# Kernel optimization log

Measured on AMD Instinct MI355X. Metric: run time of the kernel, lower is better.

Reference implementation:

```python
import jax, jax.numpy as jnp
import numpy as np

N_NODES = 100000
N_EDGES = 1600000
F_IN = 128
F_OUT = 64


def setup_inputs() -> dict:
    key = jax.random.key(0)
    k0, k1, k2, k3, k4, k5 = jax.random.split(key, 6)
    stdv = 1.0 / np.sqrt(F_OUT)
    x = jax.random.normal(k0, (N_NODES, F_IN), dtype=jnp.float32)
    edge_src = jax.random.randint(k1, (N_EDGES,), 0, N_NODES, dtype=jnp.int32)
    edge_dst = jax.random.randint(k2, (N_EDGES,), 0, N_NODES, dtype=jnp.int32)
    # normalized adjacency values (all positive, like D^-1/2 A D^-1/2 entries)
    edge_weight = jax.random.uniform(k3, (N_EDGES,), dtype=jnp.float32)
    weight = jax.random.uniform(k4, (F_IN, F_OUT), dtype=jnp.float32, minval=-stdv, maxval=stdv)
    bias = jax.random.uniform(k5, (F_OUT,), dtype=jnp.float32, minval=-stdv, maxval=stdv)
    return {"x": x, "edge_weight": edge_weight, "weight": weight, "bias": bias,
            "edge_src": edge_src, "edge_dst": edge_dst}


def reference(x, edge_weight, weight, bias, edge_src, edge_dst):
    # support = X @ W  -- dense GEMM [N, F_in] x [F_in, F_out]
    support = x @ weight
    # spmm(adj, support): adj in COO form; gather source rows, scale by edge value,
    # scatter-add into destination rows.
    msgs = support[edge_src] * edge_weight[:, None]          # [E, F_out]
    out = jax.ops.segment_sum(msgs, edge_dst, num_segments=x.shape[0])
    return out + bias
```

## Files before the change

kernel.cpp:

```cpp
#include <hip/hip_runtime.h>
#include <hip/hip_bf16.h>

#define F_IN 128
#define F_OUT 64
#define BUCKET_SHIFT 7
#define BUCKET_NODES 128
#define BUCKET_CAP 2880
#define CNT_STRIDE 16
#define NB_MAX 800
#define SCAT_CHUNK 8192
#define P1_GEMM_ROWS 64
#define LDK 136

typedef __attribute__((ext_vector_type(8))) short bf16x8;
typedef __attribute__((ext_vector_type(4))) float f32x4;

__device__ inline short bf16_bits(float f) {
  __hip_bfloat16 h = __float2bfloat16(f);
  return *reinterpret_cast<short*>(&h);
}

union Phase1Smem {
  struct { short Bs[F_OUT][LDK]; } g;
  struct { int lhist[NB_MAX]; int lcur[NB_MAX]; int ldst[SCAT_CHUNK]; } s;
};

__global__ __launch_bounds__(512, 6) void gcn_phase1_kernel(
    const float* __restrict__ x, const float* __restrict__ w,
    __hip_bfloat16* __restrict__ support,
    const int* __restrict__ esrc, const int* __restrict__ edst,
    const float* __restrict__ ew, int* __restrict__ bcount,
    int2* __restrict__ region, int n_nodes, int n_edges, int nb,
    int n_scat_blocks) {
  __shared__ Phase1Smem sm;
  const int tid = threadIdx.x;

  if ((int)blockIdx.x < n_scat_blocks) {
    const int e0 = blockIdx.x * SCAT_CHUNK;
    const int e1 = min(e0 + SCAT_CHUNK, n_edges);
    const int n_local = e1 - e0;

    for (int i = tid; i < nb; i += 512) sm.s.lhist[i] = 0;
    __syncthreads();
    for (int i = tid; i < n_local; i += 512) {
      const int d = edst[e0 + i];
      sm.s.ldst[i] = d;
      atomicAdd(&sm.s.lhist[d >> BUCKET_SHIFT], 1);
    }
    __syncthreads();
    for (int b = tid; b < nb; b += 512) {
      const int c = sm.s.lhist[b];
      sm.s.lcur[b] = c ? atomicAdd(&bcount[b * CNT_STRIDE], c) : 0;
    }
    __syncthreads();
    for (int i = tid; i < n_local; i += 512) {
      const int d = sm.s.ldst[i];
      const int b = d >> BUCKET_SHIFT;
      const int pos = atomicAdd(&sm.s.lcur[b], 1);
      if (pos < BUCKET_CAP) {
        region[(size_t)b * BUCKET_CAP + pos] =
            make_int2((esrc[e0 + i] << BUCKET_SHIFT) | (d & (BUCKET_NODES - 1)),
                      __float_as_int(ew[e0 + i]));
      }
    }
  } else {
    const int gbid = (int)blockIdx.x - n_scat_blocks;
    const int block_row = gbid * P1_GEMM_ROWS;

#pragma unroll
    for (int i = 0; i < F_IN * F_OUT / 512; ++i) {
      const int idx = tid + i * 512;
      sm.g.Bs[idx & 63][idx >> 6] = bf16_bits(w[idx]);
    }

    const int lane = tid & 63;
    const int wid = tid >> 6;
    const int wr0 = (wid >> 1) * 16;
    const int wc0 = (wid & 1) * 32;
    const int m = lane & 15;
    const int quad = lane >> 4;
    const int row = block_row + wr0 + m;

    bf16x8 afrag[4];
    if (row < n_nodes) {
      const float4* xr = (const float4*)(x + (size_t)row * F_IN);
#pragma unroll
      for (int ks = 0; ks < 4; ++ks) {
        const float4 v0 = xr[ks * 8 + quad * 2];
        const float4 v1 = xr[ks * 8 + quad * 2 + 1];
        bf16x8 a;
        a[0] = bf16_bits(v0.x); a[1] = bf16_bits(v0.y);
        a[2] = bf16_bits(v0.z); a[3] = bf16_bits(v0.w);
        a[4] = bf16_bits(v1.x); a[5] = bf16_bits(v1.y);
        a[6] = bf16_bits(v1.z); a[7] = bf16_bits(v1.w);
        afrag[ks] = a;
      }
    } else {
#pragma unroll
      for (int ks = 0; ks < 4; ++ks) afrag[ks] = (bf16x8)0;
    }
    __syncthreads();

    f32x4 acc0 = {0.f, 0.f, 0.f, 0.f};
    f32x4 acc1 = {0.f, 0.f, 0.f, 0.f};
#pragma unroll
    for (int ks = 0; ks < 4; ++ks) {
      const int ko = ks * 32 + quad * 8;
      const bf16x8 b0 = *(const bf16x8*)&sm.g.Bs[wc0 + m][ko];
      const bf16x8 b1 = *(const bf16x8*)&sm.g.Bs[wc0 + 16 + m][ko];
      acc0 = __builtin_amdgcn_mfma_f32_16x16x32_bf16(afrag[ks], b0, acc0, 0, 0, 0);
      acc1 = __builtin_amdgcn_mfma_f32_16x16x32_bf16(afrag[ks], b1, acc1, 0, 0, 0);
    }
#pragma unroll
    for (int r = 0; r < 4; ++r) {
      const int orow = block_row + wr0 + quad * 4 + r;
      if (orow < n_nodes) {
        __hip_bfloat16* op = support + (size_t)orow * F_OUT;
        op[wc0 + m]      = __float2bfloat16(acc0[r]);
        op[wc0 + 16 + m] = __float2bfloat16(acc1[r]);
      }
    }
  }
}

__global__ __launch_bounds__(512, 6) void gcn_sort_agg_kernel(
    const __hip_bfloat16* __restrict__ support,
    const int2* __restrict__ region, const int* __restrict__ bcount,
    const float* __restrict__ bias, float* __restrict__ out, int n_nodes) {
  __shared__ int2 outb[BUCKET_CAP];
  __shared__ int hist[BUCKET_NODES];
  __shared__ int nbeg[BUCKET_NODES];
  __shared__ int lcur[BUCKET_NODES];
  const int b = blockIdx.x;
  const int tid = threadIdx.x;
  const int lane = tid & 63;

  int cnt = bcount[b * CNT_STRIDE];
  cnt = (cnt < BUCKET_CAP ? cnt : BUCKET_CAP);
  const int2* reg = region + (size_t)b * BUCKET_CAP;

  for (int i = tid; i < BUCKET_NODES; i += 512) hist[i] = 0;
  __syncthreads();
  for (int i = tid; i < cnt; i += 512) {
    atomicAdd(&hist[reg[i].x & (BUCKET_NODES - 1)], 1);
  }
  __syncthreads();
  if (tid < 64) {
    const int v0 = hist[lane];
    const int v1 = hist[64 + lane];
    int s0 = v0;
#pragma unroll
    for (int off = 1; off < 64; off <<= 1) {
      const int t = __shfl_up(s0, off, 64);
      if (lane >= off) s0 += t;
    }
    const int tot0 = __shfl(s0, 63, 64);
    int s1 = v1;
#pragma unroll
    for (int off = 1; off < 64; off <<= 1) {
      const int t = __shfl_up(s1, off, 64);
      if (lane >= off) s1 += t;
    }
    s1 += tot0;
    nbeg[lane] = s0 - v0;
    nbeg[64 + lane] = s1 - v1;
    lcur[lane] = s0 - v0;
    lcur[64 + lane] = s1 - v1;
  }
  __syncthreads();
  for (int i = tid; i < cnt; i += 512) {
    const int2 p = reg[i];
    const int pos = atomicAdd(&lcur[p.x & (BUCKET_NODES - 1)], 1);
    outb[pos] = make_int2(p.x >> BUCKET_SHIFT, p.y);
  }
  __syncthreads();

  const int wid = tid >> 6;
  const int r = lane >> 4;
  const int c4 = (lane & 15) * 4;
  const ushort* sup = (const ushort*)support;
  const float4 b4 = *(const float4*)(bias + c4);
  for (int nl = wid * 16; nl < wid * 16 + 16; ++nl) {
    const int g = (b << BUCKET_SHIFT) + nl;
    if (g >= n_nodes) break;
    const int s = nbeg[nl];
    const int e = lcur[nl];
    f32x4 acc0 = {0.f, 0.f, 0.f, 0.f};
    f32x4 acc1 = {0.f, 0.f, 0.f, 0.f};
    for (int j = s; j < e; j += 8) {
      const int jr0 = j + r;
      const int jr1 = j + 4 + r;
      const bool va = jr0 < e;
      const bool vb = jr1 < e;
      const int2 m0 = outb[va ? jr0 : e - 1];
      const int2 m1 = outb[vb ? jr1 : e - 1];
      const float w0 = va ? __int_as_float(m0.y) : 0.f;
      const float w1 = vb ? __int_as_float(m1.y) : 0.f;
      const uint2 d0 = *(const uint2*)(sup + (size_t)m0.x * F_OUT + c4);
      const uint2 d1 = *(const uint2*)(sup + (size_t)m1.x * F_OUT + c4);
      acc0[0] = fmaf(__uint_as_float(d0.x << 16), w0, acc0[0]);
      acc0[1] = fmaf(__uint_as_float(d0.x & 0xffff0000u), w0, acc0[1]);
      acc0[2] = fmaf(__uint_as_float(d0.y << 16), w0, acc0[2]);
      acc0[3] = fmaf(__uint_as_float(d0.y & 0xffff0000u), w0, acc0[3]);
      acc1[0] = fmaf(__uint_as_float(d1.x << 16), w1, acc1[0]);
      acc1[1] = fmaf(__uint_as_float(d1.x & 0xffff0000u), w1, acc1[1]);
      acc1[2] = fmaf(__uint_as_float(d1.y << 16), w1, acc1[2]);
      acc1[3] = fmaf(__uint_as_float(d1.y & 0xffff0000u), w1, acc1[3]);
    }
#pragma unroll
    for (int i = 0; i < 4; ++i) {
      float v = acc0[i] + acc1[i];
      v += __shfl_xor(v, 16, 64);
      v += __shfl_xor(v, 32, 64);
      acc0[i] = v;
    }
    if (r == 0) {
      float4 o;
      o.x = acc0[0] + b4.x;
      o.y = acc0[1] + b4.y;
      o.z = acc0[2] + b4.z;
      o.w = acc0[3] + b4.w;
      *(float4*)(out + (size_t)g * F_OUT + c4) = o;
    }
  }
}

extern "C" void kernel_launch(void* const* d_in, const int* in_sizes, int n_in,
                              void* d_out, int out_size, void* d_ws, size_t ws_size,
                              hipStream_t stream) {
  const float* x    = (const float*)d_in[0];
  const float* ew   = (const float*)d_in[1];
  const float* w    = (const float*)d_in[2];
  const float* bias = (const float*)d_in[3];
  const int*   esrc = (const int*)d_in[4];
  const int*   edst = (const int*)d_in[5];
  float* out = (float*)d_out;

  const int n_nodes = in_sizes[0] / F_IN;
  const int n_edges = in_sizes[4];
  const int nb = (n_nodes + BUCKET_NODES - 1) >> BUCKET_SHIFT;

  char* ws = (char*)d_ws;
  size_t off = 0;
  auto alloc = [&](size_t bytes) {
    size_t o = off;
    off += (bytes + 255) / 256 * 256;
    return o;
  };
  const size_t off_bcount  = alloc((size_t)nb * CNT_STRIDE * sizeof(int));
  const size_t off_region  = alloc((size_t)nb * BUCKET_CAP * sizeof(int2));
  const size_t off_support = alloc((size_t)n_nodes * F_OUT * sizeof(__hip_bfloat16));
  (void)off_support;

  int*  bcount = (int*)(ws + off_bcount);
  int2* region = (int2*)(ws + off_region);
  __hip_bfloat16* support = (__hip_bfloat16*)(ws + off_support);

  const int scat_blocks = (n_edges + SCAT_CHUNK - 1) / SCAT_CHUNK;
  const int gemm_blocks = (n_nodes + P1_GEMM_ROWS - 1) / P1_GEMM_ROWS;

  hipMemsetAsync(bcount, 0, (size_t)nb * CNT_STRIDE * sizeof(int), stream);
  gcn_phase1_kernel<<<scat_blocks + gemm_blocks, 512, 0, stream>>>(
      x, w, support, esrc, edst, ew, bcount, region, n_nodes, n_edges, nb,
      scat_blocks);
  gcn_sort_agg_kernel<<<nb, 512, 0, stream>>>(support, region, bcount, bias,
                                              out, n_nodes);
}
```

Measured before the change: 181.4 us.

## Keep edges in registers, persist GEMM blocks, widen aggregation gathers

```diff
diff --git a/kernel.cpp b/kernel.cpp
--- a/kernel.cpp
+++ b/kernel.cpp
@@ -8,9 +8,12 @@
 #define BUCKET_CAP 2880
 #define CNT_STRIDE 16
 #define NB_MAX 800
-#define SCAT_CHUNK 8192
+#define SCAT_CHUNK 4096
+#define EPT 8
 #define P1_GEMM_ROWS 64
+#define N_GEMM_BLOCKS 768
 #define LDK 136
+#define SA_EPT 6
 
 typedef __attribute__((ext_vector_type(8))) short bf16x8;
 typedef __attribute__((ext_vector_type(4))) float f32x4;
@@ -22,7 +25,7 @@
 
 union Phase1Smem {
   struct { short Bs[F_OUT][LDK]; } g;
-  struct { int lhist[NB_MAX]; int lcur[NB_MAX]; int ldst[SCAT_CHUNK]; } s;
+  struct { int lhist[NB_MAX]; int lcur[NB_MAX]; } s;
 };
 
 __global__ __launch_bounds__(512, 6) void gcn_phase1_kernel(
@@ -31,21 +34,26 @@
     const int* __restrict__ esrc, const int* __restrict__ edst,
     const float* __restrict__ ew, int* __restrict__ bcount,
     int2* __restrict__ region, int n_nodes, int n_edges, int nb,
-    int n_scat_blocks) {
+    int n_scat_blocks, int ntiles) {
   __shared__ Phase1Smem sm;
   const int tid = threadIdx.x;
 
   if ((int)blockIdx.x < n_scat_blocks) {
     const int e0 = blockIdx.x * SCAT_CHUNK;
-    const int e1 = min(e0 + SCAT_CHUNK, n_edges);
-    const int n_local = e1 - e0;
+    const int n_local = min(SCAT_CHUNK, n_edges - e0);
 
     for (int i = tid; i < nb; i += 512) sm.s.lhist[i] = 0;
     __syncthreads();
-    for (int i = tid; i < n_local; i += 512) {
-      const int d = edst[e0 + i];
-      sm.s.ldst[i] = d;
-      atomicAdd(&sm.s.lhist[d >> BUCKET_SHIFT], 1);
+    int dreg[EPT];
+#pragma unroll
+    for (int p = 0; p < EPT; ++p) {
+      const int i = tid + p * 512;
+      dreg[p] = -1;
+      if (i < n_local) {
+        const int d = edst[e0 + i];
+        dreg[p] = d;
+        atomicAdd(&sm.s.lhist[d >> BUCKET_SHIFT], 1);
+      }
     }
     __syncthreads();
     for (int b = tid; b < nb; b += 512) {
@@ -53,25 +61,28 @@
       sm.s.lcur[b] = c ? atomicAdd(&bcount[b * CNT_STRIDE], c) : 0;
     }
     __syncthreads();
-    for (int i = tid; i < n_local; i += 512) {
-      const int d = sm.s.ldst[i];
-      const int b = d >> BUCKET_SHIFT;
-      const int pos = atomicAdd(&sm.s.lcur[b], 1);
-      if (pos < BUCKET_CAP) {
-        region[(size_t)b * BUCKET_CAP + pos] =
-            make_int2((esrc[e0 + i] << BUCKET_SHIFT) | (d & (BUCKET_NODES - 1)),
-                      __float_as_int(ew[e0 + i]));
+#pragma unroll
+    for (int p = 0; p < EPT; ++p) {
+      const int i = tid + p * 512;
+      const int d = dreg[p];
+      if (d >= 0) {
+        const int b = d >> BUCKET_SHIFT;
+        const int pos = atomicAdd(&sm.s.lcur[b], 1);
+        if (pos < BUCKET_CAP) {
+          region[(size_t)b * BUCKET_CAP + pos] = make_int2(
+              (esrc[e0 + i] << BUCKET_SHIFT) | (d & (BUCKET_NODES - 1)),
+              __float_as_int(ew[e0 + i]));
+        }
       }
     }
   } else {
     const int gbid = (int)blockIdx.x - n_scat_blocks;
-    const int block_row = gbid * P1_GEMM_ROWS;
-
 #pragma unroll
     for (int i = 0; i < F_IN * F_OUT / 512; ++i) {
       const int idx = tid + i * 512;
       sm.g.Bs[idx & 63][idx >> 6] = bf16_bits(w[idx]);
     }
+    __syncthreads();
 
     const int lane = tid & 63;
     const int wid = tid >> 6;
@@ -79,45 +90,48 @@
     const int wc0 = (wid & 1) * 32;
     const int m = lane & 15;
     const int quad = lane >> 4;
-    const int row = block_row + wr0 + m;
-
-    bf16x8 afrag[4];
-    if (row < n_nodes) {
-      const float4* xr = (const float4*)(x + (size_t)row * F_IN);
+
+    for (int t = gbid; t < ntiles; t += N_GEMM_BLOCKS) {
+      const int block_row = t * P1_GEMM_ROWS;
+      const int row = block_row + wr0 + m;
+
+      bf16x8 afrag[4];
+      if (row < n_nodes) {
+        const float4* xr = (const float4*)(x + (size_t)row * F_IN);
+#pragma unroll
+        for (int ks = 0; ks < 4; ++ks) {
+          const float4 v0 = xr[ks * 8 + quad * 2];
+          const float4 v1 = xr[ks * 8 + quad * 2 + 1];
+          bf16x8 a;
+          a[0] = bf16_bits(v0.x); a[1] = bf16_bits(v0.y);
+          a[2] = bf16_bits(v0.z); a[3] = bf16_bits(v0.w);
+          a[4] = bf16_bits(v1.x); a[5] = bf16_bits(v1.y);
+          a[6] = bf16_bits(v1.z); a[7] = bf16_bits(v1.w);
+          afrag[ks] = a;
+        }
+      } else {
+#pragma unroll
+        for (int ks = 0; ks < 4; ++ks) afrag[ks] = (bf16x8)0;
+      }
+
+      f32x4 acc0 = {0.f, 0.f, 0.f, 0.f};
+      f32x4 acc1 = {0.f, 0.f, 0.f, 0.f};
 #pragma unroll
       for (int ks = 0; ks < 4; ++ks) {
-        const float4 v0 = xr[ks * 8 + quad * 2];
-        const float4 v1 = xr[ks * 8 + quad * 2 + 1];
-        bf16x8 a;
-        a[0] = bf16_bits(v0.x); a[1] = bf16_bits(v0.y);
-        a[2] = bf16_bits(v0.z); a[3] = bf16_bits(v0.w);
-        a[4] = bf16_bits(v1.x); a[5] = bf16_bits(v1.y);
-        a[6] = bf16_bits(v1.z); a[7] = bf16_bits(v1.w);
-        afrag[ks] = a;
-      }
-    } else {
-#pragma unroll
-      for (int ks = 0; ks < 4; ++ks) afrag[ks] = (bf16x8)0;
-    }
-    __syncthreads();
-
-    f32x4 acc0 = {0.f, 0.f, 0.f, 0.f};
-    f32x4 acc1 = {0.f, 0.f, 0.f, 0.f};
-#pragma unroll
-    for (int ks = 0; ks < 4; ++ks) {
-      const int ko = ks * 32 + quad * 8;
-      const bf16x8 b0 = *(const bf16x8*)&sm.g.Bs[wc0 + m][ko];
-      const bf16x8 b1 = *(const bf16x8*)&sm.g.Bs[wc0 + 16 + m][ko];
-      acc0 = __builtin_amdgcn_mfma_f32_16x16x32_bf16(afrag[ks], b0, acc0, 0, 0, 0);
-      acc1 = __builtin_amdgcn_mfma_f32_16x16x32_bf16(afrag[ks], b1, acc1, 0, 0, 0);
-    }
-#pragma unroll
-    for (int r = 0; r < 4; ++r) {
-      const int orow = block_row + wr0 + quad * 4 + r;
-      if (orow < n_nodes) {
-        __hip_bfloat16* op = support + (size_t)orow * F_OUT;
-        op[wc0 + m]      = __float2bfloat16(acc0[r]);
-        op[wc0 + 16 + m] = __float2bfloat16(acc1[r]);
+        const int ko = ks * 32 + quad * 8;
+        const bf16x8 b0 = *(const bf16x8*)&sm.g.Bs[wc0 + m][ko];
+        const bf16x8 b1 = *(const bf16x8*)&sm.g.Bs[wc0 + 16 + m][ko];
+        acc0 = __builtin_amdgcn_mfma_f32_16x16x32_bf16(afrag[ks], b0, acc0, 0, 0, 0);
+        acc1 = __builtin_amdgcn_mfma_f32_16x16x32_bf16(afrag[ks], b1, acc1, 0, 0, 0);
+      }
+#pragma unroll
+      for (int r = 0; r < 4; ++r) {
+        const int orow = block_row + wr0 + quad * 4 + r;
+        if (orow < n_nodes) {
+          __hip_bfloat16* op = support + (size_t)orow * F_OUT;
+          op[wc0 + m]      = __float2bfloat16(acc0[r]);
+          op[wc0 + 16 + m] = __float2bfloat16(acc1[r]);
+        }
       }
     }
   }
@@ -128,26 +142,36 @@
     const int2* __restrict__ region, const int* __restrict__ bcount,
     const float* __restrict__ bias, float* __restrict__ out, int n_nodes) {
   __shared__ int2 outb[BUCKET_CAP];
-  __shared__ int hist[BUCKET_NODES];
+  __shared__ int hist4[4][BUCKET_NODES];
   __shared__ int nbeg[BUCKET_NODES];
   __shared__ int lcur[BUCKET_NODES];
   const int b = blockIdx.x;
   const int tid = threadIdx.x;
   const int lane = tid & 63;
+  const int hq = (tid >> 7) & 3;
 
   int cnt = bcount[b * CNT_STRIDE];
   cnt = (cnt < BUCKET_CAP ? cnt : BUCKET_CAP);
   const int2* reg = region + (size_t)b * BUCKET_CAP;
 
-  for (int i = tid; i < BUCKET_NODES; i += 512) hist[i] = 0;
-  __syncthreads();
-  for (int i = tid; i < cnt; i += 512) {
-    atomicAdd(&hist[reg[i].x & (BUCKET_NODES - 1)], 1);
+  for (int i = tid; i < 4 * BUCKET_NODES; i += 512) ((int*)hist4)[i] = 0;
+  __syncthreads();
+  int2 ereg[SA_EPT];
+#pragma unroll
+  for (int p = 0; p < SA_EPT; ++p) {
+    const int i = tid + p * 512;
+    ereg[p].x = -1;
+    if (i < cnt) {
+      ereg[p] = reg[i];
+      atomicAdd(&hist4[hq][ereg[p].x & (BUCKET_NODES - 1)], 1);
+    }
   }
   __syncthreads();
   if (tid < 64) {
-    const int v0 = hist[lane];
-    const int v1 = hist[64 + lane];
+    const int v0 = hist4[0][lane] + hist4[1][lane] + hist4[2][lane] +
+                   hist4[3][lane];
+    const int l1 = 64 + lane;
+    const int v1 = hist4[0][l1] + hist4[1][l1] + hist4[2][l1] + hist4[3][l1];
     int s0 = v0;
 #pragma unroll
     for (int off = 1; off < 64; off <<= 1) {
@@ -163,64 +187,64 @@
     }
     s1 += tot0;
     nbeg[lane] = s0 - v0;
-    nbeg[64 + lane] = s1 - v1;
+    nbeg[l1] = s1 - v1;
     lcur[lane] = s0 - v0;
-    lcur[64 + lane] = s1 - v1;
-  }
-  __syncthreads();
-  for (int i = tid; i < cnt; i += 512) {
-    const int2 p = reg[i];
-    const int pos = atomicAdd(&lcur[p.x & (BUCKET_NODES - 1)], 1);
-    outb[pos] = make_int2(p.x >> BUCKET_SHIFT, p.y);
+    lcur[l1] = s1 - v1;
+  }
+  __syncthreads();
+#pragma unroll
+  for (int p = 0; p < SA_EPT; ++p) {
+    if (ereg[p].x >= 0) {
+      const int pos = atomicAdd(&lcur[ereg[p].x & (BUCKET_NODES - 1)], 1);
+      outb[pos] = make_int2(ereg[p].x >> BUCKET_SHIFT, ereg[p].y);
+    }
   }
   __syncthreads();
 
   const int wid = tid >> 6;
-  const int r = lane >> 4;
-  const int c4 = (lane & 15) * 4;
+  const int r = lane >> 3;
+  const int cg = lane & 7;
   const ushort* sup = (const ushort*)support;
-  const float4 b4 = *(const float4*)(bias + c4);
+  const float4 bb0 = *(const float4*)(bias + cg * 8);
+  const float4 bb1 = *(const float4*)(bias + cg * 8 + 4);
   for (int nl = wid * 16; nl < wid * 16 + 16; ++nl) {
     const int g = (b << BUCKET_SHIFT) + nl;
     if (g >= n_nodes) break;
     const int s = nbeg[nl];
     const int e = lcur[nl];
-    f32x4 acc0 = {0.f, 0.f, 0.f, 0.f};
-    f32x4 acc1 = {0.f, 0.f, 0.f, 0.f};
+    float acc[8] = {0.f, 0.f, 0.f, 0.f, 0.f, 0.f, 0.f, 0.f};
     for (int j = s; j < e; j += 8) {
-      const int jr0 = j + r;
-      const int jr1 = j + 4 + r;
-      const bool va = jr0 < e;
-      const bool vb = jr1 < e;
-      const int2 m0 = outb[va ? jr0 : e - 1];
-      const int2 m1 = outb[vb ? jr1 : e - 1];
-      const float w0 = va ? __int_as_float(m0.y) : 0.f;
-      const float w1 = vb ? __int_as_float(m1.y) : 0.f;
-      const uint2 d0 = *(const uint2*)(sup + (size_t)m0.x * F_OUT + c4);
-      const uint2 d1 = *(const uint2*)(sup + (size_t)m1.x * F_OUT + c4);
-      acc0[0] = fmaf(__uint_as_float(d0.x << 16), w0, acc0[0]);
-      acc0[1] = fmaf(__uint_as_float(d0.x & 0xffff0000u), w0, acc0[1]);
-      acc0[2] = fmaf(__uint_as_float(d0.y << 16), w0, acc0[2]);
-      acc0[3] = fmaf(__uint_as_float(d0.y & 0xffff0000u), w0, acc0[3]);
-      acc1[0] = fmaf(__uint_as_float(d1.x << 16), w1, acc1[0]);
-      acc1[1] = fmaf(__uint_as_float(d1.x & 0xffff0000u), w1, acc1[1]);
-      acc1[2] = fmaf(__uint_as_float(d1.y << 16), w1, acc1[2]);
-      acc1[3] = fmaf(__uint_as_float(d1.y & 0xffff0000u), w1, acc1[3]);
-    }
-#pragma unroll
-    for (int i = 0; i < 4; ++i) {
-      float v = acc0[i] + acc1[i];
+      const int jr = j + r;
+      const bool valid = jr < e;
+      const int2 meta = outb[valid ? jr : e - 1];
+      const float wv = valid ? __int_as_float(meta.y) : 0.f;
+      const uint4 d = *(const uint4*)(sup + (size_t)meta.x * F_OUT + cg * 8);
+      acc[0] = fmaf(__uint_as_float(d.x << 16), wv, acc[0]);
+      acc[1] = fmaf(__uint_as_float(d.x & 0xffff0000u), wv, acc[1]);
+      acc[2] = fmaf(__uint_as_float(d.y << 16), wv, acc[2]);
+      acc[3] = fmaf(__uint_as_float(d.y & 0xffff0000u), wv, acc[3]);
+      acc[4] = fmaf(__uint_as_float(d.z << 16), wv, acc[4]);
+      acc[5] = fmaf(__uint_as_float(d.z & 0xffff0000u), wv, acc[5]);
+      acc[6] = fmaf(__uint_as_float(d.w << 16), wv, acc[6]);
+      acc[7] = fmaf(__uint_as_float(d.w & 0xffff0000u), wv, acc[7]);
+    }
+#pragma unroll
+    for (int i = 0; i < 8; ++i) {
+      float v = acc[i];
+      v += __shfl_xor(v, 8, 64);
       v += __shfl_xor(v, 16, 64);
       v += __shfl_xor(v, 32, 64);
-      acc0[i] = v;
+      acc[i] = v;
     }
     if (r == 0) {
-      float4 o;
-      o.x = acc0[0] + b4.x;
-      o.y = acc0[1] + b4.y;
-      o.z = acc0[2] + b4.z;
-      o.w = acc0[3] + b4.w;
-      *(float4*)(out + (size_t)g * F_OUT + c4) = o;
+      float* op = out + (size_t)g * F_OUT + cg * 8;
+      float4 o0, o1;
+      o0.x = acc[0] + bb0.x; o0.y = acc[1] + bb0.y;
+      o0.z = acc[2] + bb0.z; o0.w = acc[3] + bb0.w;
+      o1.x = acc[4] + bb1.x; o1.y = acc[5] + bb1.y;
+      o1.z = acc[6] + bb1.z; o1.w = acc[7] + bb1.w;
+      *(float4*)op = o0;
+      *(float4*)(op + 4) = o1;
     }
   }
 }
@@ -257,12 +281,12 @@
   __hip_bfloat16* support = (__hip_bfloat16*)(ws + off_support);
 
   const int scat_blocks = (n_edges + SCAT_CHUNK - 1) / SCAT_CHUNK;
-  const int gemm_blocks = (n_nodes + P1_GEMM_ROWS - 1) / P1_GEMM_ROWS;
+  const int ntiles = (n_nodes + P1_GEMM_ROWS - 1) / P1_GEMM_ROWS;
 
   hipMemsetAsync(bcount, 0, (size_t)nb * CNT_STRIDE * sizeof(int), stream);
-  gcn_phase1_kernel<<<scat_blocks + gemm_blocks, 512, 0, stream>>>(
+  gcn_phase1_kernel<<<scat_blocks + N_GEMM_BLOCKS, 512, 0, stream>>>(
       x, w, support, esrc, edst, ew, bcount, region, n_nodes, n_edges, nb,
-      scat_blocks);
+      scat_blocks, ntiles);
   gcn_sort_agg_kernel<<<nb, 512, 0, stream>>>(support, region, bcount, bias,
                                               out, n_nodes);
 }
```

Measured after the change: 207.2 us. 14.2% more time.
